# Performance work log

Measured on AMD Instinct MI355X. Metric: run time of the kernel, lower is better.

The kernel has to match this reference:

```python
import jax, jax.numpy as jnp
import numpy as np

MARGIN = 1.0


def setup_inputs() -> dict:
    key = jax.random.key(0)
    k1, k2, k3, k4 = jax.random.split(key, 4)
    B, H, W = 512, 128, 128
    return {
        "entropy": jax.random.normal(k1, (B, H, W), dtype=jnp.float32),
        "alignment": jax.random.normal(k2, (B, H, W), dtype=jnp.float32),
        "curvature": jax.random.normal(k3, (B, H, W), dtype=jnp.float32),
        "targets": jax.random.randint(k4, (B,), 0, 10, dtype=jnp.int64),
    }


def _pairwise_mean_sq_dist(x):
    # x: [B, H, W] -> D[i, j] = mean((x_i - x_j)**2) over HxW, shape [B, B]
    B = x.shape[0]
    xf = x.reshape(B, -1)                      # [B, D]
    Dflat = xf.shape[1]
    sq = jnp.sum(xf * xf, axis=1)              # [B]
    gram = jnp.einsum("bd,cd->bc", xf, xf)     # [B, B], compute-bound GEMM
    return (sq[:, None] + sq[None, :] - 2.0 * gram) / Dflat


def reference(entropy, alignment, curvature, targets):
    B = targets.shape[0]
    # total structural distance = sum of per-field mean squared differences
    dist = (_pairwise_mean_sq_dist(entropy)
            + _pairwise_mean_sq_dist(alignment)
            + _pairwise_mean_sq_dist(curvature))        # [B, B]
    labels_equal = targets[:, None] == targets[None, :]  # [B, B] bool
    # positive pairs: distance; negative pairs: hinge clamp(margin - d, 0)
    per_pair = jnp.where(labels_equal, dist, jnp.maximum(MARGIN - dist, 0.0))
    # only i < j pairs, as in the original double loop
    upper = jnp.triu(jnp.ones((B, B), dtype=bool), k=1)
    num_pairs = B * (B - 1) // 2
    return jnp.sum(jnp.where(upper, per_pair, 0.0)) / num_pairs
```

## Files before the change

kernel.cpp:

```cpp
#include <hip/hip_runtime.h>
#include <hip/hip_bf16.h>
#include <stdint.h>

typedef __attribute__((ext_vector_type(4))) float f32x4;
typedef __attribute__((ext_vector_type(8))) unsigned short ushort8;
typedef __attribute__((ext_vector_type(2))) unsigned long long ull2;

#define BSZ 512
#define KTOT 49152
#define KSPLIT 48
#define KCHUNK 1024
#define BK 128
#define NKSTEP (KCHUNK / BK)
#define NTILE 10
#define TSIZE (128 * 128)
#define SKEW 5
#define NPAIRS 130816.0f

__device__ __forceinline__ float bf2f(ushort u) {
    return __uint_as_float(((uint32_t)u) << 16);
}

__device__ __forceinline__ ushort f2bf(float f) {
    uint32_t u = __float_as_uint(f);
    uint32_t r = (u + 0x7fffu + ((u >> 16) & 1u)) >> 16;
    return (ushort)r;
}

__device__ __forceinline__ void gload_lds16(const uint8_t* g, uint8_t* l) {
    __builtin_amdgcn_global_load_lds(
        (const __attribute__((address_space(1))) uint32_t*)g,
        (__attribute__((address_space(3))) uint32_t*)l, 16, 0, 0);
}

__global__ __launch_bounds__(256) void convert_kernel(
    const float* __restrict__ e, const float* __restrict__ a,
    const float* __restrict__ c, uint8_t* __restrict__ W,
    int* __restrict__ ticket) {
    if (blockIdx.x == 0 && threadIdx.x == 0) *ticket = 0;
    const int g = blockIdx.x * 256 + threadIdx.x;
    const int E = g * 8;
    const int f = E >> 23;
    const int rem = E & 8388607;
    const int row = rem >> 14, col = rem & 16383;
    const float* src = (f == 0) ? e : (f == 1 ? a : c);
    float4 v0 = reinterpret_cast<const float4*>(src + rem)[0];
    float4 v1 = reinterpret_cast<const float4*>(src + rem)[1];
    uint lo = __builtin_amdgcn_cvt_pk_fp8_f32(v0.x, v0.y, 0, false);
    lo = __builtin_amdgcn_cvt_pk_fp8_f32(v0.z, v0.w, lo, true);
    uint hi = __builtin_amdgcn_cvt_pk_fp8_f32(v1.x, v1.y, 0, false);
    hi = __builtin_amdgcn_cvt_pk_fp8_f32(v1.z, v1.w, hi, true);
    const int k = f * 16384 + col;
    const int H = k >> 6, s = (k >> 5) & 1, q = (k >> 3) & 3;
    const size_t phys = (size_t)row * KTOT + H * 64 + q * 16 + s * 8;
    uint2 w = {lo, hi};
    *reinterpret_cast<uint2*>(&W[phys]) = w;
}

__global__ __launch_bounds__(256, 2) void gemm_kernel(
    const uint8_t* __restrict__ W, ushort* __restrict__ P, float* __restrict__ Pd) {
    const int tile = blockIdx.x / KSPLIT;
    const int ks   = blockIdx.x % KSPLIT;
    int ti = 0, rem = tile;
    while (rem >= 4 - ti) { rem -= 4 - ti; ++ti; }
    const int tj = ti + rem;
    const bool diag = (ti == tj);
    const int brow = ti * 128, bcol = tj * 128;
    const int kbase = ks * KCHUNK;

    __shared__ uint8_t As[128 * 128];
    __shared__ uint8_t Bs[128 * 128];

    const int t = threadIdx.x;
    const int lane = t & 63, wid = t >> 6;
    const int wr = (wid >> 1) * 64, wc = (wid & 1) * 64;
    const bool skipw = diag && (wr == 64) && (wc == 0);

    const int grow = t >> 3, s = t & 7;
    const int swz = (s ^ (grow & 7)) * 16;
    const uint8_t* pa = W + (size_t)(brow + grow) * KTOT + kbase + swz;
    const uint8_t* pb = W + (size_t)(bcol + grow) * KTOT + kbase + swz;
    uint8_t* la = &As[t * 16];
    uint8_t* lb = &Bs[t * 16];

    const f32x4 zero = {0.f, 0.f, 0.f, 0.f};
    f32x4 acc[4][4];
#pragma unroll
    for (int m = 0; m < 4; ++m)
#pragma unroll
        for (int n = 0; n < 4; ++n) acc[m][n] = zero;

#pragma unroll 1
    for (int kt = 0; kt < NKSTEP; ++kt) {
        const int kk = kt * BK;
#pragma unroll
        for (int i = 0; i < 4; ++i)
            gload_lds16(pa + (size_t)(i * 32) * KTOT + kk, la + i * 4096);
        if (!diag) {
#pragma unroll
            for (int i = 0; i < 4; ++i)
                gload_lds16(pb + (size_t)(i * 32) * KTOT + kk, lb + i * 4096);
        }
        __syncthreads();
        if (!skipw) {
            const uint8_t* Bsrc = diag ? As : Bs;
#pragma unroll
            for (int half = 0; half < 2; ++half) {
                ull2 af[4], bfv[4];
                const int kq = half * 4 + (lane >> 4);
#pragma unroll
                for (int m = 0; m < 4; ++m) {
                    const int row = wr + m * 16 + (lane & 15);
                    const int gg = kq ^ (row & 7);
                    af[m] = *reinterpret_cast<const ull2*>(&As[row * 128 + gg * 16]);
                }
#pragma unroll
                for (int n = 0; n < 4; ++n) {
                    const int row = wc + n * 16 + (lane & 15);
                    const int gg = kq ^ (row & 7);
                    bfv[n] = *reinterpret_cast<const ull2*>(&Bsrc[row * 128 + gg * 16]);
                }
#pragma unroll
                for (int m = 0; m < 4; ++m)
#pragma unroll
                    for (int n = 0; n < 4; ++n) {
                        acc[m][n] = __builtin_amdgcn_mfma_f32_16x16x32_fp8_fp8(
                            (long long)af[m][0], (long long)bfv[n][0], acc[m][n], 0, 0, 0);
                        acc[m][n] = __builtin_amdgcn_mfma_f32_16x16x32_fp8_fp8(
                            (long long)af[m][1], (long long)bfv[n][1], acc[m][n], 0, 0, 0);
                    }
            }
        }
        __syncthreads();
    }

    if (!skipw) {
        ushort* Pk = P + (size_t)(tile * KSPLIT + ks) * TSIZE;
        const int ci = (lane >> 4) * 4, cj = lane & 15;
#pragma unroll
        for (int m = 0; m < 4; ++m)
#pragma unroll
            for (int n = 0; n < 4; ++n)
#pragma unroll
                for (int r = 0; r < 4; ++r) {
                    const int li = wr + m * 16 + ci + r;
                    const int lj = wc + n * 16 + cj;
                    const int pr = (li + SKEW * ks) & 127;
                    Pk[pr * 128 + lj] = f2bf(acc[m][n][r]);
                    if (diag && li == lj)
                        Pd[ks * BSZ + brow + li] = acc[m][n][r];
                }
    }
}

__global__ __launch_bounds__(256) void pairred_kernel(
    const ushort* __restrict__ P, const float* __restrict__ Pd,
    const int* __restrict__ tg, float* __restrict__ LP,
    int* __restrict__ ticket, float* __restrict__ out) {
    __shared__ float sd[BSZ];
    __shared__ float red[4];
    __shared__ int slast;
    const int t = threadIdx.x;
    float d0 = 0.f, d1 = 0.f;
#pragma unroll 8
    for (int k = 0; k < KSPLIT; ++k) {
        d0 += Pd[k * BSZ + t];
        d1 += Pd[k * BSZ + t + 256];
    }
    sd[t] = d0;
    sd[t + 256] = d1;
    __syncthreads();

    const int gid = blockIdx.x * 256 + t;
    const int i = gid >> 6;
    const int j0 = (gid & 63) * 8;
    float local = 0.f;
    if (j0 + 7 > i) {
        const int ti2 = i >> 7, tj2 = j0 >> 7;
        const int tidx = (ti2 * (9 - ti2)) / 2 + (tj2 - ti2);
        const int li = i & 127, lj0 = j0 & 127;
        const ushort* base = P + (size_t)tidx * KSPLIT * TSIZE + lj0;
        float sum[8];
#pragma unroll
        for (int u = 0; u < 8; ++u) sum[u] = 0.f;
        for (int k = 0; k < KSPLIT; ++k) {
            const int pr = (li + SKEW * k) & 127;
            ushort8 v = *reinterpret_cast<const ushort8*>(base + (size_t)k * TSIZE + pr * 128);
#pragma unroll
            for (int u = 0; u < 8; ++u) sum[u] += bf2f(v[u]);
        }
        const float di = sd[i];
        const int lbl = tg[i];
#pragma unroll
        for (int u = 0; u < 8; ++u) {
            const int j = j0 + u;
            if (j > i) {
                const float d = (di + sd[j] - 2.f * sum[u]) * (1.f / 16384.f);
                local += (lbl == tg[j]) ? d : fmaxf(1.f - d, 0.f);
            }
        }
    }
#pragma unroll
    for (int off = 32; off; off >>= 1) local += __shfl_down(local, off, 64);
    const int lane = t & 63, wid = t >> 6;
    if (lane == 0) red[wid] = local;
    __syncthreads();
    if (t == 0) {
        LP[blockIdx.x] = red[0] + red[1] + red[2] + red[3];
        __threadfence();
        slast = (atomicAdd(ticket, 1) == 127);
    }
    __syncthreads();
    if (slast && t < 128) {
        __threadfence();
        float v = LP[t];
#pragma unroll
        for (int off = 32; off; off >>= 1) v += __shfl_down(v, off, 64);
        if (t == 0) red[0] = v;
        __syncthreads();
        if (t == 64 && lane == 0) red[1] = v;
        __syncthreads();
        if (t == 0) out[0] = (red[0] + red[1]) * (1.f / NPAIRS);
    }
}

extern "C" void kernel_launch(void* const* d_in, const int* in_sizes, int n_in,
                              void* d_out, int out_size, void* d_ws, size_t ws_size,
                              hipStream_t stream) {
    const float* e  = (const float*)d_in[0];
    const float* a  = (const float*)d_in[1];
    const float* c  = (const float*)d_in[2];
    const int*   tg = (const int*)d_in[3];

    uint8_t* W   = (uint8_t*)d_ws;
    ushort*  P   = (ushort*)(W + (size_t)BSZ * KTOT);
    float*   Pd  = (float*)(P + (size_t)NTILE * KSPLIT * TSIZE);
    float*   LP  = Pd + KSPLIT * BSZ;
    int*     ticket = (int*)(LP + 128);
    float*   out = (float*)d_out;

    convert_kernel<<<dim3(12288), dim3(256), 0, stream>>>(e, a, c, W, ticket);
    gemm_kernel<<<dim3(NTILE * KSPLIT), dim3(256), 0, stream>>>(W, P, Pd);
    pairred_kernel<<<dim3(128), dim3(256), 0, stream>>>(P, Pd, tg, LP, ticket, out);
}
```

Baseline: 50.73 us.

## Use 256x256 GEMM tiles with fp8 split-K partials and a separate K-reduce kernel

The Gram GEMM moves from ten 128x128 upper-triangle tiles to three 256x256 tiles, with 512-thread blocks, split-K doubled to 96 and 512-wide K chunks. Split-K partials are stored as fp8 instead of bf16, which cuts partial-buffer traffic. A new kernel sums the partials over K into a dense float Gram buffer, and the pair-loss kernel then reads single floats. Storing partials in fp8 costs accuracy. The launch bounds (512, 4) together with 128 accumulator floats per thread risk register spills, and the change adds one kernel launch.

```diff
diff --git a/kernel.cpp b/kernel.cpp
--- a/kernel.cpp
+++ b/kernel.cpp
@@ -3,29 +3,18 @@
 #include <stdint.h>
 
 typedef __attribute__((ext_vector_type(4))) float f32x4;
-typedef __attribute__((ext_vector_type(8))) unsigned short ushort8;
 typedef __attribute__((ext_vector_type(2))) unsigned long long ull2;
 
 #define BSZ 512
 #define KTOT 49152
-#define KSPLIT 48
-#define KCHUNK 1024
+#define KSPLIT 96
+#define KCHUNK 512
 #define BK 128
 #define NKSTEP (KCHUNK / BK)
-#define NTILE 10
-#define TSIZE (128 * 128)
+#define BM 256
+#define TSIZE (BM * BM)
 #define SKEW 5
 #define NPAIRS 130816.0f
-
-__device__ __forceinline__ float bf2f(ushort u) {
-    return __uint_as_float(((uint32_t)u) << 16);
-}
-
-__device__ __forceinline__ ushort f2bf(float f) {
-    uint32_t u = __float_as_uint(f);
-    uint32_t r = (u + 0x7fffu + ((u >> 16) & 1u)) >> 16;
-    return (ushort)r;
-}
 
 __device__ __forceinline__ void gload_lds16(const uint8_t* g, uint8_t* l) {
     __builtin_amdgcn_global_load_lds(
@@ -57,24 +46,23 @@
     *reinterpret_cast<uint2*>(&W[phys]) = w;
 }
 
-__global__ __launch_bounds__(256, 2) void gemm_kernel(
-    const uint8_t* __restrict__ W, ushort* __restrict__ P, float* __restrict__ Pd) {
-    const int tile = blockIdx.x / KSPLIT;
-    const int ks   = blockIdx.x % KSPLIT;
-    int ti = 0, rem = tile;
-    while (rem >= 4 - ti) { rem -= 4 - ti; ++ti; }
-    const int tj = ti + rem;
-    const bool diag = (ti == tj);
-    const int brow = ti * 128, bcol = tj * 128;
+__global__ __launch_bounds__(512, 4) void gemm_kernel(
+    const uint8_t* __restrict__ W, uint8_t* __restrict__ P, float* __restrict__ Pd) {
+    const int tt = blockIdx.x / KSPLIT;
+    const int ks = blockIdx.x % KSPLIT;
+    const int ti = (tt == 2) ? 1 : 0;
+    const int tj = (tt == 0) ? 0 : 1;
+    const bool diag = (tt != 1);
+    const int brow = ti * BM, bcol = tj * BM;
     const int kbase = ks * KCHUNK;
 
-    __shared__ uint8_t As[128 * 128];
-    __shared__ uint8_t Bs[128 * 128];
+    __shared__ uint8_t As[BM * 128];
+    __shared__ uint8_t Bs[BM * 128];
 
     const int t = threadIdx.x;
     const int lane = t & 63, wid = t >> 6;
-    const int wr = (wid >> 1) * 64, wc = (wid & 1) * 64;
-    const bool skipw = diag && (wr == 64) && (wc == 0);
+    const int wm = wid >> 2, wn = wid & 3;
+    const bool skipw = diag && (wm == 1) && (wn < 2);
 
     const int grow = t >> 3, s = t & 7;
     const int swz = (s ^ (grow & 7)) * 16;
@@ -84,9 +72,9 @@
     uint8_t* lb = &Bs[t * 16];
 
     const f32x4 zero = {0.f, 0.f, 0.f, 0.f};
-    f32x4 acc[4][4];
-#pragma unroll
-    for (int m = 0; m < 4; ++m)
+    f32x4 acc[8][4];
+#pragma unroll
+    for (int m = 0; m < 8; ++m)
 #pragma unroll
         for (int n = 0; n < 4; ++n) acc[m][n] = zero;
 
@@ -95,33 +83,33 @@
         const int kk = kt * BK;
 #pragma unroll
         for (int i = 0; i < 4; ++i)
-            gload_lds16(pa + (size_t)(i * 32) * KTOT + kk, la + i * 4096);
+            gload_lds16(pa + (size_t)(i * 64) * KTOT + kk, la + i * 8192);
         if (!diag) {
 #pragma unroll
             for (int i = 0; i < 4; ++i)
-                gload_lds16(pb + (size_t)(i * 32) * KTOT + kk, lb + i * 4096);
+                gload_lds16(pb + (size_t)(i * 64) * KTOT + kk, lb + i * 8192);
         }
         __syncthreads();
         if (!skipw) {
             const uint8_t* Bsrc = diag ? As : Bs;
 #pragma unroll
             for (int half = 0; half < 2; ++half) {
-                ull2 af[4], bfv[4];
+                ull2 af[8], bfv[4];
                 const int kq = half * 4 + (lane >> 4);
 #pragma unroll
-                for (int m = 0; m < 4; ++m) {
-                    const int row = wr + m * 16 + (lane & 15);
+                for (int m = 0; m < 8; ++m) {
+                    const int row = wm * 128 + m * 16 + (lane & 15);
                     const int gg = kq ^ (row & 7);
                     af[m] = *reinterpret_cast<const ull2*>(&As[row * 128 + gg * 16]);
                 }
 #pragma unroll
                 for (int n = 0; n < 4; ++n) {
-                    const int row = wc + n * 16 + (lane & 15);
+                    const int row = wn * 64 + n * 16 + (lane & 15);
                     const int gg = kq ^ (row & 7);
                     bfv[n] = *reinterpret_cast<const ull2*>(&Bsrc[row * 128 + gg * 16]);
                 }
 #pragma unroll
-                for (int m = 0; m < 4; ++m)
+                for (int m = 0; m < 8; ++m)
 #pragma unroll
                     for (int n = 0; n < 4; ++n) {
                         acc[m][n] = __builtin_amdgcn_mfma_f32_16x16x32_fp8_fp8(
@@ -135,26 +123,50 @@
     }
 
     if (!skipw) {
-        ushort* Pk = P + (size_t)(tile * KSPLIT + ks) * TSIZE;
+        uint8_t* Pk = P + ((size_t)tt * KSPLIT + ks) * TSIZE;
         const int ci = (lane >> 4) * 4, cj = lane & 15;
 #pragma unroll
-        for (int m = 0; m < 4; ++m)
+        for (int m = 0; m < 8; ++m)
 #pragma unroll
             for (int n = 0; n < 4; ++n)
 #pragma unroll
                 for (int r = 0; r < 4; ++r) {
-                    const int li = wr + m * 16 + ci + r;
-                    const int lj = wc + n * 16 + cj;
-                    const int pr = (li + SKEW * ks) & 127;
-                    Pk[pr * 128 + lj] = f2bf(acc[m][n][r]);
+                    const int li = wm * 128 + m * 16 + ci + r;
+                    const int lj = wn * 64 + n * 16 + cj;
+                    const int pr = (li + SKEW * ks) & 255;
+                    const float v = acc[m][n][r];
+                    const uint pk = __builtin_amdgcn_cvt_pk_fp8_f32(v, v, 0, false);
+                    Pk[pr * BM + lj] = (uint8_t)(pk & 0xff);
                     if (diag && li == lj)
-                        Pd[ks * BSZ + brow + li] = acc[m][n][r];
+                        Pd[ks * BSZ + brow + li] = v;
                 }
     }
 }
 
-__global__ __launch_bounds__(256) void pairred_kernel(
-    const ushort* __restrict__ P, const float* __restrict__ Pd,
+__global__ __launch_bounds__(128) void reducek_kernel(
+    const uint8_t* __restrict__ P, float* __restrict__ G) {
+    const int t = threadIdx.x;
+    const int tile  = blockIdx.x >> 7;
+    const int chunk = blockIdx.x & 127;
+    const int li  = chunk * 2 + (t >> 6);
+    const int ljc = (t & 63) * 4;
+    float s0 = 0.f, s1 = 0.f, s2 = 0.f, s3 = 0.f;
+    const uint8_t* base = P + (size_t)tile * KSPLIT * TSIZE + ljc;
+#pragma unroll 8
+    for (int k = 0; k < KSPLIT; ++k) {
+        const int pr = (li + SKEW * k) & 255;
+        const uint v = *reinterpret_cast<const uint*>(base + (size_t)k * TSIZE + pr * BM);
+        s0 += __builtin_amdgcn_cvt_f32_fp8(v, 0);
+        s1 += __builtin_amdgcn_cvt_f32_fp8(v, 1);
+        s2 += __builtin_amdgcn_cvt_f32_fp8(v, 2);
+        s3 += __builtin_amdgcn_cvt_f32_fp8(v, 3);
+    }
+    float4 g = {s0, s1, s2, s3};
+    *reinterpret_cast<float4*>(&G[(size_t)tile * TSIZE + li * BM + ljc]) = g;
+}
+
+__global__ __launch_bounds__(256) void pairfin_kernel(
+    const float* __restrict__ G, const float* __restrict__ Pd,
     const int* __restrict__ tg, float* __restrict__ LP,
     int* __restrict__ ticket, float* __restrict__ out) {
     __shared__ float sd[BSZ];
@@ -176,26 +188,20 @@
     const int j0 = (gid & 63) * 8;
     float local = 0.f;
     if (j0 + 7 > i) {
-        const int ti2 = i >> 7, tj2 = j0 >> 7;
-        const int tidx = (ti2 * (9 - ti2)) / 2 + (tj2 - ti2);
-        const int li = i & 127, lj0 = j0 & 127;
-        const ushort* base = P + (size_t)tidx * KSPLIT * TSIZE + lj0;
-        float sum[8];
-#pragma unroll
-        for (int u = 0; u < 8; ++u) sum[u] = 0.f;
-        for (int k = 0; k < KSPLIT; ++k) {
-            const int pr = (li + SKEW * k) & 127;
-            ushort8 v = *reinterpret_cast<const ushort8*>(base + (size_t)k * TSIZE + pr * 128);
-#pragma unroll
-            for (int u = 0; u < 8; ++u) sum[u] += bf2f(v[u]);
-        }
+        const int ti2 = i >> 8, tj2 = j0 >> 8;
+        const int tidx = ti2 + tj2;
+        const int li = i & 255, lj0 = j0 & 255;
+        const float* g = G + (size_t)tidx * TSIZE + li * BM + lj0;
+        float4 g0 = reinterpret_cast<const float4*>(g)[0];
+        float4 g1 = reinterpret_cast<const float4*>(g)[1];
+        float gv[8] = {g0.x, g0.y, g0.z, g0.w, g1.x, g1.y, g1.z, g1.w};
         const float di = sd[i];
         const int lbl = tg[i];
 #pragma unroll
         for (int u = 0; u < 8; ++u) {
             const int j = j0 + u;
             if (j > i) {
-                const float d = (di + sd[j] - 2.f * sum[u]) * (1.f / 16384.f);
+                const float d = (di + sd[j] - 2.f * gv[u]) * (1.f / 16384.f);
                 local += (lbl == tg[j]) ? d : fmaxf(1.f - d, 0.f);
             }
         }
@@ -233,13 +239,15 @@
     const int*   tg = (const int*)d_in[3];
 
     uint8_t* W   = (uint8_t*)d_ws;
-    ushort*  P   = (ushort*)(W + (size_t)BSZ * KTOT);
-    float*   Pd  = (float*)(P + (size_t)NTILE * KSPLIT * TSIZE);
+    uint8_t* P   = W + (size_t)BSZ * KTOT;
+    float*   G   = (float*)(P + (size_t)3 * KSPLIT * TSIZE);
+    float*   Pd  = G + (size_t)3 * TSIZE;
     float*   LP  = Pd + KSPLIT * BSZ;
     int*     ticket = (int*)(LP + 128);
     float*   out = (float*)d_out;
 
     convert_kernel<<<dim3(12288), dim3(256), 0, stream>>>(e, a, c, W, ticket);
-    gemm_kernel<<<dim3(NTILE * KSPLIT), dim3(256), 0, stream>>>(W, P, Pd);
-    pairred_kernel<<<dim3(128), dim3(256), 0, stream>>>(P, Pd, tg, LP, ticket, out);
-}
+    gemm_kernel<<<dim3(3 * KSPLIT), dim3(512), 0, stream>>>(W, P, Pd);
+    reducek_kernel<<<dim3(384), dim3(128), 0, stream>>>(P, G);
+    pairfin_kernel<<<dim3(128), dim3(256), 0, stream>>>(G, Pd, tg, LP, ticket, out);
+}
```

After: 107.9 us. 2.13x slower.

## Split split-K partial reduction into a separate wide kernel before pair finalization

Applied to the files above, without the earlier changes.

The split-K reduction over the 48 bf16 partial tiles moves out of the 128-block pair-reduction kernel into a new 320-block kernel that writes fp32 Gram tiles to workspace. The finalize kernel then reads one fp32 value per pair instead of looping over 48 partials. This spreads the reduction's memory traffic across more blocks and CUs, which was underused with only 128 blocks. The cost is one more kernel launch plus an extra write and read of the reduced Gram tiles.

```diff
diff --git a/kernel.cpp b/kernel.cpp
--- a/kernel.cpp
+++ b/kernel.cpp
@@ -3,7 +3,6 @@
 #include <stdint.h>
 
 typedef __attribute__((ext_vector_type(4))) float f32x4;
-typedef __attribute__((ext_vector_type(8))) unsigned short ushort8;
 typedef __attribute__((ext_vector_type(2))) unsigned long long ull2;
 
 #define BSZ 512
@@ -153,8 +152,28 @@
     }
 }
 
-__global__ __launch_bounds__(256) void pairred_kernel(
-    const ushort* __restrict__ P, const float* __restrict__ Pd,
+__global__ __launch_bounds__(256) void reducek_kernel(
+    const ushort* __restrict__ P, float* __restrict__ G) {
+    const int t = threadIdx.x;
+    const int tile  = blockIdx.x >> 5;
+    const int chunk = blockIdx.x & 31;
+    const int li  = chunk * 4 + (t >> 6);
+    const int ljq = (t & 63) * 2;
+    float s0 = 0.f, s1 = 0.f;
+    const ushort* base = P + (size_t)tile * KSPLIT * TSIZE + ljq;
+#pragma unroll 8
+    for (int k = 0; k < KSPLIT; ++k) {
+        const int pr = (li + SKEW * k) & 127;
+        const uint v = *reinterpret_cast<const uint*>(base + (size_t)k * TSIZE + pr * 128);
+        s0 += bf2f((ushort)(v & 0xffff));
+        s1 += bf2f((ushort)(v >> 16));
+    }
+    float2 g = {s0, s1};
+    *reinterpret_cast<float2*>(&G[(size_t)tile * TSIZE + li * 128 + ljq]) = g;
+}
+
+__global__ __launch_bounds__(256) void pairfin_kernel(
+    const float* __restrict__ G, const float* __restrict__ Pd,
     const int* __restrict__ tg, float* __restrict__ LP,
     int* __restrict__ ticket, float* __restrict__ out) {
     __shared__ float sd[BSZ];
@@ -179,23 +198,17 @@
         const int ti2 = i >> 7, tj2 = j0 >> 7;
         const int tidx = (ti2 * (9 - ti2)) / 2 + (tj2 - ti2);
         const int li = i & 127, lj0 = j0 & 127;
-        const ushort* base = P + (size_t)tidx * KSPLIT * TSIZE + lj0;
-        float sum[8];
-#pragma unroll
-        for (int u = 0; u < 8; ++u) sum[u] = 0.f;
-        for (int k = 0; k < KSPLIT; ++k) {
-            const int pr = (li + SKEW * k) & 127;
-            ushort8 v = *reinterpret_cast<const ushort8*>(base + (size_t)k * TSIZE + pr * 128);
-#pragma unroll
-            for (int u = 0; u < 8; ++u) sum[u] += bf2f(v[u]);
-        }
+        const float* g = G + (size_t)tidx * TSIZE + li * 128 + lj0;
+        float4 g0 = reinterpret_cast<const float4*>(g)[0];
+        float4 g1 = reinterpret_cast<const float4*>(g)[1];
+        float gv[8] = {g0.x, g0.y, g0.z, g0.w, g1.x, g1.y, g1.z, g1.w};
         const float di = sd[i];
         const int lbl = tg[i];
 #pragma unroll
         for (int u = 0; u < 8; ++u) {
             const int j = j0 + u;
             if (j > i) {
-                const float d = (di + sd[j] - 2.f * sum[u]) * (1.f / 16384.f);
+                const float d = (di + sd[j] - 2.f * gv[u]) * (1.f / 16384.f);
                 local += (lbl == tg[j]) ? d : fmaxf(1.f - d, 0.f);
             }
         }
@@ -234,12 +247,14 @@
 
     uint8_t* W   = (uint8_t*)d_ws;
     ushort*  P   = (ushort*)(W + (size_t)BSZ * KTOT);
-    float*   Pd  = (float*)(P + (size_t)NTILE * KSPLIT * TSIZE);
+    float*   G   = (float*)(P + (size_t)NTILE * KSPLIT * TSIZE);
+    float*   Pd  = G + (size_t)NTILE * TSIZE;
     float*   LP  = Pd + KSPLIT * BSZ;
     int*     ticket = (int*)(LP + 128);
     float*   out = (float*)d_out;
 
     convert_kernel<<<dim3(12288), dim3(256), 0, stream>>>(e, a, c, W, ticket);
     gemm_kernel<<<dim3(NTILE * KSPLIT), dim3(256), 0, stream>>>(W, P, Pd);
-    pairred_kernel<<<dim3(128), dim3(256), 0, stream>>>(P, Pd, tg, LP, ticket, out);
-}
+    reducek_kernel<<<dim3(320), dim3(256), 0, stream>>>(P, G);
+    pairfin_kernel<<<dim3(128), dim3(256), 0, stream>>>(G, Pd, tg, LP, ticket, out);
+}
```

New measurement: 51.60 us. No clear change (+1.7%).
